# Performance work log

Measured on AMD Instinct MI355X. Metric: run time of the kernel, lower is better.

## Reference

```python
import jax, jax.numpy as jnp
import numpy as np

B, F, S = 2, 512, 1024
E = 4
I = 1024          # intermediate = 2 * features
K = 3             # conv kernel size
INIT_SCALE = 1.0
EPS = 1e-5
SLOPE = 0.02


def setup_inputs() -> dict:
    key = jax.random.key(0)
    k = jax.random.split(key, 6)
    inp = jax.random.normal(k[0], (B, F, S), jnp.float32)
    divisor = (jnp.arange(S, dtype=jnp.float32) + 1.0).reshape(1, 1, S)
    w0_gate = jax.random.normal(k[1], (E, F, 1), jnp.float32) * (F ** -0.5)
    w0 = jax.random.normal(k[2], (E, F, 3 * I), jnp.float32) * (F ** -0.5)
    w1 = jax.random.normal(k[3], (3 * I, I, K), jnp.float32) * ((I * K) ** -0.5)
    w2_gate = jax.random.normal(k[4], (E, I, 1), jnp.float32) * (I ** -0.5)
    w2 = jax.random.normal(k[5], (E, I, F), jnp.float32) * (I ** -0.5)
    return {"inp": inp, "divisor": divisor, "w0_gate": w0_gate, "w0": w0,
            "w1": w1, "w2_gate": w2_gate, "w2": w2}


def _norm(x):
    # channel norm over dim 1: subtract mean, divide by scaled L2 norm
    x = x - jnp.mean(x, axis=1, keepdims=True)
    n = jnp.sqrt(jnp.sum(x * x, axis=1, keepdims=True)) * (x.shape[1] ** -0.5)
    return x / (n + EPS)


def _moe(x, gate, w):
    # x: [B,F,S]; gate: [E,F,1]; w: [E,F,D]
    logits = jnp.einsum('bfs,ef->bes', x, gate[:, :, 0])          # [B,E,S]
    gates = jax.nn.softmax(logits, axis=1)
    idx = jnp.argmax(logits, axis=1)                              # [B,S]
    one_hot = jax.nn.one_hot(idx, w.shape[0], dtype=x.dtype)      # [B,S,E]
    # straight-through gumbel-style gate: hard one-hot fwd, soft grad
    gumbel = jnp.transpose(one_hot, (0, 2, 1)) - jax.lax.stop_gradient(gates) + gates  # [B,E,S]
    xs = jnp.transpose(x, (0, 2, 1))                              # [B,S,F]
    out = jnp.zeros((x.shape[0], x.shape[2], w.shape[2]), x.dtype)
    for e in range(w.shape[0]):  # small fixed expert count
        mask = one_hot[:, :, e][:, :, None]                       # [B,S,1]
        out = out + mask * ((xs * gumbel[:, e, :, None]) @ w[e])
    loss = jnp.sum(jnp.mean(gates, axis=(0, 2)) * jnp.mean(one_hot, axis=(0, 1)))
    return loss, jnp.transpose(out, (0, 2, 1))                    # [B,D,S]


def _conv1d(x, w, causal_pad):
    if causal_pad and w.shape[-1] > 1:
        x = jnp.pad(x, ((0, 0), (0, 0), (w.shape[-1] - 1, 0)))
    return jax.lax.conv_general_dilated(
        x, w, window_strides=(1,), padding='VALID',
        dimension_numbers=('NCH', 'OIH', 'NCH'), feature_group_count=1)


def reference(inp, divisor, w0_gate, w0, w1, w2_gate, w2):
    loss0, h = _moe(inp, w0_gate, w0)                 # [B,3I,S]
    depth, scale, shift = jnp.split(h, 3, axis=1)     # each [B,I,S]
    cum = jnp.cumsum(depth, axis=-1)
    h = jax.nn.leaky_relu(_norm(cum / divisor * scale + shift), SLOPE)
    h = _conv1d(h, w1, causal_pad=True)               # [B,3I,S]
    s0, s1, sh = jnp.split(h, 3, axis=1)
    h = jax.nn.leaky_relu(_norm(s0 * s1 + sh), SLOPE)
    loss1, out = _moe(h, w2_gate, w2)                 # [B,F,S]
    return out * INIT_SCALE, loss0 + loss1
```

## Files before the change

### kernel.cpp

```cpp
#include <hip/hip_runtime.h>
#include <hip/hip_bf16.h>

#define SDIM 1024

typedef float f32x4 __attribute__((ext_vector_type(4)));
typedef short short8 __attribute__((ext_vector_type(8)));

__device__ __forceinline__ unsigned short f2bf(float f) {
    __hip_bfloat16 h = __float2bfloat16(f);
    return *reinterpret_cast<unsigned short*>(&h);
}
__device__ __forceinline__ float bf2f(unsigned short u) {
    return __uint_as_float(((unsigned int)u) << 16);
}

__global__ void init_acc_kernel(float* acc) {
    int t = threadIdx.x;
    if (t < 16) acc[t] = 0.0f;
}

__global__ __launch_bounds__(256) void transpose_cvt_split(
    const float* __restrict__ in, unsigned short* __restrict__ oh,
    unsigned short* __restrict__ ol, int R, int C, size_t sliceStride)
{
    __shared__ float t[32][33];
    int slice = blockIdx.z;
    int c0 = blockIdx.x * 32, r0 = blockIdx.y * 32;
    int tid = threadIdx.x;
    int cc = tid & 31, r8 = tid >> 5;
    const float* ip = in + slice * sliceStride;
    #pragma unroll
    for (int k = 0; k < 4; ++k) {
        int r = r8 + k * 8;
        t[r][cc] = ip[(size_t)(r0 + r) * C + c0 + cc];
    }
    __syncthreads();
    #pragma unroll
    for (int k = 0; k < 4; ++k) {
        int rr = r8 + k * 8;
        float v = t[cc][rr];
        unsigned short hi = f2bf(v);
        unsigned short lo = f2bf(v - bf2f(hi));
        size_t o = slice * sliceStride + (size_t)(c0 + rr) * R + r0 + cc;
        oh[o] = hi; ol[o] = lo;
    }
}

__global__ __launch_bounds__(256) void transpose_cvt(
    const float* __restrict__ in, unsigned short* __restrict__ out,
    int R, int C, size_t sliceStride)
{
    __shared__ float t[32][33];
    int slice = blockIdx.z;
    int c0 = blockIdx.x * 32, r0 = blockIdx.y * 32;
    int tid = threadIdx.x;
    int cc = tid & 31, r8 = tid >> 5;
    const float* ip = in + slice * sliceStride;
    unsigned short* op = out + slice * sliceStride;
    #pragma unroll
    for (int k = 0; k < 4; ++k) {
        int r = r8 + k * 8;
        t[r][cc] = ip[(size_t)(r0 + r) * C + c0 + cc];
    }
    __syncthreads();
    #pragma unroll
    for (int k = 0; k < 4; ++k) {
        int rr = r8 + k * 8;
        op[(size_t)(c0 + rr) * R + r0 + cc] = f2bf(t[cc][rr]);
    }
}

__global__ __launch_bounds__(256) void w1cvt_split_kernel(
    const float* __restrict__ w1, unsigned short* __restrict__ wh,
    unsigned short* __restrict__ wl)
{
    int t = blockIdx.x * 256 + threadIdx.x;
    int o = t >> 10, i = t & 1023;
    const float* p = w1 + (size_t)o * 3072 + i * 3;
    #pragma unroll
    for (int k = 0; k < 3; ++k) {
        float v = p[k];
        unsigned short hi = f2bf(v);
        unsigned short lo = f2bf(v - bf2f(hi));
        size_t off = (size_t)k * 3145728 + (size_t)o * 1024 + i;
        wh[off] = hi; wl[off] = lo;
    }
}

__global__ __launch_bounds__(256) void gate_kernel(
    const float* __restrict__ x, const float* __restrict__ wg,
    int* __restrict__ idx, float* __restrict__ acc, int accBase)
{
    __shared__ float wgs[4 * 512];
    __shared__ float part[32][4][9];
    __shared__ float la[8];
    int tid = threadIdx.x;
    if (tid < 8) la[tid] = 0.f;
    for (int l = tid; l < 2048; l += 256) wgs[l] = wg[l];
    __syncthreads();
    int t0 = blockIdx.x * 8;
    int b = t0 >> 10, s0 = t0 & 1023;
    int sl = tid & 7, fg = tid >> 3;
    float l0 = 0.f, l1 = 0.f, l2 = 0.f, l3 = 0.f;
    for (int f = fg; f < 512; f += 32) {
        float xv = x[((size_t)b * 512 + f) * SDIM + s0 + sl];
        l0 += xv * wgs[f];
        l1 += xv * wgs[512 + f];
        l2 += xv * wgs[1024 + f];
        l3 += xv * wgs[1536 + f];
    }
    part[fg][0][sl] = l0; part[fg][1][sl] = l1;
    part[fg][2][sl] = l2; part[fg][3][sl] = l3;
    __syncthreads();
    for (int h = 16; h >= 1; h >>= 1) {
        if (fg < h) {
            #pragma unroll
            for (int e = 0; e < 4; ++e) part[fg][e][sl] += part[fg + h][e][sl];
        }
        __syncthreads();
    }
    if (fg == 0) {
        float L[4] = {part[0][0][sl], part[0][1][sl], part[0][2][sl], part[0][3][sl]};
        float m = fmaxf(fmaxf(L[0], L[1]), fmaxf(L[2], L[3]));
        float e0 = expf(L[0] - m), e1 = expf(L[1] - m), e2 = expf(L[2] - m), e3 = expf(L[3] - m);
        float inv = 1.0f / (e0 + e1 + e2 + e3);
        int best = 0; float bv = L[0];
        if (L[1] > bv) { bv = L[1]; best = 1; }
        if (L[2] > bv) { bv = L[2]; best = 2; }
        if (L[3] > bv) { bv = L[3]; best = 3; }
        idx[t0 + sl] = best;
        atomicAdd(&la[0], e0 * inv);
        atomicAdd(&la[1], e1 * inv);
        atomicAdd(&la[2], e2 * inv);
        atomicAdd(&la[3], e3 * inv);
        atomicAdd(&la[4 + best], 1.0f);
    }
    __syncthreads();
    if (tid < 8) atomicAdd(&acc[accBase + tid], la[tid]);
}

__global__ __launch_bounds__(1024) void sort_kernel(
    const int* __restrict__ idx, int* __restrict__ perm, int* __restrict__ eSorted)
{
    int b = blockIdx.x;
    int tid = threadIdx.x;
    int lane = tid & 63, w = tid >> 6;
    int e = idx[(b << 10) + tid];
    __shared__ int wcnt[16][4];
    __shared__ int woff[16][4];
    int r = 0;
    unsigned long long lt = (1ull << lane) - 1ull;
    #pragma unroll
    for (int eo = 0; eo < 4; ++eo) {
        unsigned long long m = __ballot(e == eo);
        if (lane == 0) wcnt[w][eo] = __popcll(m);
        if (e == eo) r = __popcll(m & lt);
    }
    __syncthreads();
    if (tid == 0) {
        int baseAcc = 0;
        for (int eo = 0; eo < 4; ++eo)
            for (int ww = 0; ww < 16; ++ww) { woff[ww][eo] = baseAcc; baseAcc += wcnt[ww][eo]; }
    }
    __syncthreads();
    int pos = woff[w][e] + r;
    perm[(b << 10) + pos] = tid;
    eSorted[(b << 10) + pos] = e;
}

__global__ __launch_bounds__(256) void moe_split_kernel(
    const unsigned short* __restrict__ base, unsigned int XH, unsigned int XL,
    unsigned int WH, unsigned int WL,
    const int* __restrict__ perm, const int* __restrict__ eSorted,
    float* __restrict__ out, int Fdim, int Ddim)
{
    __shared__ unsigned short lds[768 * 32];
    int id = blockIdx.x;
    int chunk = gridDim.x >> 3;
    int wg = (id & 7) * chunk + (id >> 3);
    int t0 = (wg & 15) * 128;
    int d0 = (wg >> 4) * 64;
    int b = t0 >> 10, s0 = t0 & 1023;
    int tid = threadIdx.x;
    int lane = tid & 63;
    int lm = lane & 15, q = lane >> 4;
    int wid = tid >> 6;
    int wm = (wid >> 1) * 32, wn = (wid & 1) * 64;

    unsigned int goH[6], goL[6];
    int ldH[6], ldL[6];
    #pragma unroll
    for (int t = 0; t < 6; ++t) {
        int cl = tid + t * 256;
        int row = cl >> 2, p = cl & 3;
        int rh, rl;
        unsigned int off;
        if (row < 128) {
            int tj = perm[(b << 10) + s0 + row];
            off = (unsigned int)(((b << 10) + tj) * Fdim + p * 8);
            goH[t] = XH + off; goL[t] = XL + off;
            rh = row; rl = row + 128;
        } else {
            int R = row - 128;
            int e = R >> 6, dl = R & 63;
            off = (unsigned int)((e * Ddim + d0 + dl) * Fdim + p * 8);
            goH[t] = WH + off; goL[t] = WL + off;
            rh = 256 + R; rl = 512 + R;
        }
        ldH[t] = rh * 32 + ((p ^ ((rh >> 1) & 3)) << 3);
        ldL[t] = rl * 32 + ((p ^ ((rl >> 1) & 3)) << 3);
    }

    int bofH[4], bofL[4], aofH[4][2], aofL[4][2];
    #pragma unroll
    for (int fn = 0; fn < 4; ++fn) {
        int rh = wn + fn * 16 + lm, rl = rh + 128;
        bofH[fn] = rh * 32 + ((q ^ ((rh >> 1) & 3)) << 3);
        bofL[fn] = rl * 32 + ((q ^ ((rl >> 1) & 3)) << 3);
    }
    #pragma unroll
    for (int e = 0; e < 4; ++e)
        #pragma unroll
        for (int fm = 0; fm < 2; ++fm) {
            int rh = 256 + e * 64 + wm + fm * 16 + lm;
            int rl = rh + 256;
            aofH[e][fm] = rh * 32 + ((q ^ ((rh >> 1) & 3)) << 3);
            aofL[e][fm] = rl * 32 + ((q ^ ((rl >> 1) & 3)) << 3);
        }

    int eidx[4], sv[4];
    #pragma unroll
    for (int fn = 0; fn < 4; ++fn) {
        int sl = (b << 10) + s0 + wn + fn * 16 + lm;
        eidx[fn] = eSorted[sl];
        sv[fn]   = perm[sl];
    }
    bool presF[4][4], presE[4];
    #pragma unroll
    for (int e = 0; e < 4; ++e) {
        presE[e] = false;
        #pragma unroll
        for (int fn = 0; fn < 4; ++fn) {
            presF[e][fn] = __any(eidx[fn] == e);
            presE[e] = presE[e] || presF[e][fn];
        }
    }

    f32x4 acc[2][4];
    #pragma unroll
    for (int fm = 0; fm < 2; ++fm)
        #pragma unroll
        for (int fn = 0; fn < 4; ++fn)
            acc[fm][fn] = (f32x4){0.f, 0.f, 0.f, 0.f};

    const short8 z = {0, 0, 0, 0, 0, 0, 0, 0};

    for (int f0 = 0; f0 < Fdim; f0 += 32) {
        short8 vh[6], vl[6];
        #pragma unroll
        for (int t = 0; t < 6; ++t) vh[t] = *(const short8*)(base + goH[t] + f0);
        #pragma unroll
        for (int t = 0; t < 6; ++t) vl[t] = *(const short8*)(base + goL[t] + f0);
        __syncthreads();
        #pragma unroll
        for (int t = 0; t < 6; ++t) {
            *(short8*)(lds + ldH[t]) = vh[t];
            *(short8*)(lds + ldL[t]) = vl[t];
        }
        __syncthreads();

        short8 bh[4], bl[4];
        #pragma unroll
        for (int fn = 0; fn < 4; ++fn) {
            bh[fn] = *(const short8*)(lds + bofH[fn]);
            bl[fn] = *(const short8*)(lds + bofL[fn]);
        }
        #pragma unroll
        for (int e = 0; e < 4; ++e) {
            if (presE[e]) {
                short8 ah[2], al[2];
                #pragma unroll
                for (int fm = 0; fm < 2; ++fm) {
                    ah[fm] = *(const short8*)(lds + aofH[e][fm]);
                    al[fm] = *(const short8*)(lds + aofL[e][fm]);
                }
                #pragma unroll
                for (int fn = 0; fn < 4; ++fn) {
                    if (presF[e][fn]) {
                        short8 bmH = (eidx[fn] == e) ? bh[fn] : z;
                        short8 bmL = (eidx[fn] == e) ? bl[fn] : z;
                        #pragma unroll
                        for (int fm = 0; fm < 2; ++fm) {
                            acc[fm][fn] = __builtin_amdgcn_mfma_f32_16x16x32_bf16(ah[fm], bmH, acc[fm][fn], 0, 0, 0);
                            acc[fm][fn] = __builtin_amdgcn_mfma_f32_16x16x32_bf16(ah[fm], bmL, acc[fm][fn], 0, 0, 0);
                            acc[fm][fn] = __builtin_amdgcn_mfma_f32_16x16x32_bf16(al[fm], bmH, acc[fm][fn], 0, 0, 0);
                        }
                    }
                }
            }
        }
    }

    #pragma unroll
    for (int fm = 0; fm < 2; ++fm)
        #pragma unroll
        for (int fn = 0; fn < 4; ++fn) {
            int d = d0 + wm + fm * 16 + q * 4;
            float* op = out + ((size_t)b * Ddim + d) * SDIM + sv[fn];
            #pragma unroll
            for (int r = 0; r < 4; ++r)
                op[(size_t)r * SDIM] = acc[fm][fn][r];
        }
}

__global__ __launch_bounds__(256) void conv_split_kernel(
    const unsigned short* __restrict__ base, unsigned int GH, unsigned int GL,
    unsigned int WH, unsigned int WL, float* __restrict__ co)
{
    __shared__ unsigned short lds[864 * 32];
    int id = blockIdx.x;
    int wg = (id & 7) * 64 + (id >> 3);
    int t0 = (wg & 15) * 128;
    int o0 = (wg >> 4) * 96;
    int b = t0 >> 10, s0 = t0 & 1023;
    int tid = threadIdx.x;
    int lane = tid & 63;
    int lm = lane & 15, q = lane >> 4;
    int wid = tid >> 6;
    int wm = (wid >> 1) * 48, wn = (wid & 1) * 64;

    unsigned int goH[7], goL[7];
    int ldH[7], ldL[7], act[7];
    #pragma unroll
    for (int t = 0; t < 7; ++t) {
        int cl = tid + t * 256;
        int row = cl >> 2, p = cl & 3;
        int rh, rl;
        if (row < 144) { rh = row; rl = row + 144; }
        else { int R = row - 144; rh = 288 + R; rl = 576 + R; }
        ldH[t] = rh * 32 + ((p ^ ((rh >> 1) & 3)) << 3);
        ldL[t] = rl * 32 + ((p ^ ((rl >> 1) & 3)) << 3);
        act[t] = 0; goH[t] = 0; goL[t] = 0;
        if (cl < 1728) {
            if (row < 144) {
                int s = s0 - 2 + row;
                if (s >= 0 && s < 1024) {
                    act[t] = 1;
                    unsigned int off = ((unsigned int)((b << 10) + s) << 10) + p * 8;
                    goH[t] = GH + off; goL[t] = GL + off;
                } else if (s < 0) {
                    act[t] = 2;
                }
            } else {
                int R = row - 144;
                int k = R / 96, ol = R - k * 96;
                act[t] = 1;
                unsigned int off = (unsigned int)k * 3145728u + ((unsigned int)(o0 + ol) << 10) + p * 8;
                goH[t] = WH + off; goL[t] = WL + off;
            }
        }
    }

    int aofH[3][3], aofL[3][3], bofH[3][4], bofL[3][4];
    #pragma unroll
    for (int k = 0; k < 3; ++k) {
        #pragma unroll
        for (int fm = 0; fm < 3; ++fm) {
            int R = k * 96 + wm + fm * 16 + lm;
            int rh = 288 + R, rl = 576 + R;
            aofH[k][fm] = rh * 32 + ((q ^ ((rh >> 1) & 3)) << 3);
            aofL[k][fm] = rl * 32 + ((q ^ ((rl >> 1) & 3)) << 3);
        }
        #pragma unroll
        for (int fn = 0; fn < 4; ++fn) {
            int rh = wn + fn * 16 + lm + k;
            int rl = rh + 144;
            bofH[k][fn] = rh * 32 + ((q ^ ((rh >> 1) & 3)) << 3);
            bofL[k][fn] = rl * 32 + ((q ^ ((rl >> 1) & 3)) << 3);
        }
    }

    f32x4 acc[3][4];
    #pragma unroll
    for (int fm = 0; fm < 3; ++fm)
        #pragma unroll
        for (int fn = 0; fn < 4; ++fn)
            acc[fm][fn] = (f32x4){0.f, 0.f, 0.f, 0.f};

    const short8 z = {0, 0, 0, 0, 0, 0, 0, 0};

    #pragma unroll
    for (int t = 0; t < 7; ++t)
        if (act[t] == 2) { *(short8*)(lds + ldH[t]) = z; *(short8*)(lds + ldL[t]) = z; }

    for (int i0 = 0; i0 < 1024; i0 += 32) {
        short8 vh[7], vl[7];
        #pragma unroll
        for (int t = 0; t < 7; ++t) vh[t] = (act[t] == 1) ? *(const short8*)(base + goH[t] + i0) : z;
        #pragma unroll
        for (int t = 0; t < 7; ++t) vl[t] = (act[t] == 1) ? *(const short8*)(base + goL[t] + i0) : z;
        __syncthreads();
        #pragma unroll
        for (int t = 0; t < 7; ++t)
            if (act[t] == 1) {
                *(short8*)(lds + ldH[t]) = vh[t];
                *(short8*)(lds + ldL[t]) = vl[t];
            }
        __syncthreads();

        #pragma unroll
        for (int k = 0; k < 3; ++k) {
            short8 ah[3], al[3], bh[4], bl[4];
            #pragma unroll
            for (int fm = 0; fm < 3; ++fm) {
                ah[fm] = *(const short8*)(lds + aofH[k][fm]);
                al[fm] = *(const short8*)(lds + aofL[k][fm]);
            }
            #pragma unroll
            for (int fn = 0; fn < 4; ++fn) {
                bh[fn] = *(const short8*)(lds + bofH[k][fn]);
                bl[fn] = *(const short8*)(lds + bofL[k][fn]);
            }
            #pragma unroll
            for (int fm = 0; fm < 3; ++fm)
                #pragma unroll
                for (int fn = 0; fn < 4; ++fn) {
                    acc[fm][fn] = __builtin_amdgcn_mfma_f32_16x16x32_bf16(ah[fm], bh[fn], acc[fm][fn], 0, 0, 0);
                    acc[fm][fn] = __builtin_amdgcn_mfma_f32_16x16x32_bf16(ah[fm], bl[fn], acc[fm][fn], 0, 0, 0);
                    acc[fm][fn] = __builtin_amdgcn_mfma_f32_16x16x32_bf16(al[fm], bh[fn], acc[fm][fn], 0, 0, 0);
                }
        }
    }

    #pragma unroll
    for (int fm = 0; fm < 3; ++fm)
        #pragma unroll
        for (int fn = 0; fn < 4; ++fn) {
            int o = o0 + wm + fm * 16 + q * 4;
            int s = s0 + wn + fn * 16 + lm;
            float* op = co + ((size_t)b * 3072 + o) * SDIM + s;
            #pragma unroll
            for (int r = 0; r < 4; ++r)
                op[(size_t)r * SDIM] = acc[fm][fn][r];
        }
}

__global__ __launch_bounds__(256) void moe_kernel(
    const unsigned short* __restrict__ xT, const unsigned short* __restrict__ wT,
    const int* __restrict__ perm, const int* __restrict__ eSorted,
    float* __restrict__ out, int Fdim, int Ddim)
{
    __shared__ unsigned short lds[384 * 32];
    int id = blockIdx.x;
    int chunk = gridDim.x >> 3;
    int wg = (id & 7) * chunk + (id >> 3);
    int t0 = (wg & 15) * 128;
    int d0 = (wg >> 4) * 64;
    int b = t0 >> 10, s0 = t0 & 1023;
    int tid = threadIdx.x;
    int lane = tid & 63, wid = tid >> 6;
    int lm = lane & 15, q = lane >> 4;
    int wm = (wid >> 1) * 32, wn = (wid & 1) * 64;

    const unsigned short* gsrc[6];
    int ldst[6];
    #pragma unroll
    for (int t = 0; t < 6; ++t) {
        int cl = tid + t * 256;
        int row = cl >> 2, p = cl & 3;
        int pr;
        if (row < 128) {
            int tj = perm[(b << 10) + s0 + row];
            gsrc[t] = xT + (size_t)((b << 10) + tj) * Fdim + p * 8;
            pr = row;
        } else {
            int R = row - 128;
            int e = R >> 6, dl = R & 63;
            gsrc[t] = wT + (size_t)(e * Ddim + d0 + dl) * Fdim + p * 8;
            pr = 128 + R;
        }
        ldst[t] = pr * 32 + ((p ^ ((pr >> 1) & 3)) << 3);
    }

    int bof[4], aof[4][2];
    #pragma unroll
    for (int fn = 0; fn < 4; ++fn) {
        int row = wn + fn * 16 + lm;
        bof[fn] = row * 32 + ((q ^ ((row >> 1) & 3)) << 3);
    }
    #pragma unroll
    for (int e = 0; e < 4; ++e)
        #pragma unroll
        for (int fm = 0; fm < 2; ++fm) {
            int R = 128 + e * 64 + wm + fm * 16 + lm;
            aof[e][fm] = R * 32 + ((q ^ ((R >> 1) & 3)) << 3);
        }

    int eidx[4], sv[4];
    #pragma unroll
    for (int fn = 0; fn < 4; ++fn) {
        int sl = (b << 10) + s0 + wn + fn * 16 + lm;
        eidx[fn] = eSorted[sl];
        sv[fn]   = perm[sl];
    }
    bool presF[4][4], presE[4];
    #pragma unroll
    for (int e = 0; e < 4; ++e) {
        presE[e] = false;
        #pragma unroll
        for (int fn = 0; fn < 4; ++fn) {
            presF[e][fn] = __any(eidx[fn] == e);
            presE[e] = presE[e] || presF[e][fn];
        }
    }

    f32x4 acc[2][4];
    #pragma unroll
    for (int fm = 0; fm < 2; ++fm)
        #pragma unroll
        for (int fn = 0; fn < 4; ++fn)
            acc[fm][fn] = (f32x4){0.f, 0.f, 0.f, 0.f};

    const short8 z = {0, 0, 0, 0, 0, 0, 0, 0};

    for (int f0 = 0; f0 < Fdim; f0 += 32) {
        short8 v[6];
        #pragma unroll
        for (int t = 0; t < 6; ++t)
            v[t] = *(const short8*)(gsrc[t] + f0);
        __syncthreads();
        #pragma unroll
        for (int t = 0; t < 6; ++t)
            *(short8*)(lds + ldst[t]) = v[t];
        __syncthreads();

        short8 bf[4];
        #pragma unroll
        for (int fn = 0; fn < 4; ++fn)
            bf[fn] = *(const short8*)(lds + bof[fn]);
        #pragma unroll
        for (int e = 0; e < 4; ++e) {
            if (presE[e]) {
                short8 af[2];
                #pragma unroll
                for (int fm = 0; fm < 2; ++fm)
                    af[fm] = *(const short8*)(lds + aof[e][fm]);
                #pragma unroll
                for (int fn = 0; fn < 4; ++fn) {
                    if (presF[e][fn]) {
                        short8 bm = (eidx[fn] == e) ? bf[fn] : z;
                        #pragma unroll
                        for (int fm = 0; fm < 2; ++fm)
                            acc[fm][fn] = __builtin_amdgcn_mfma_f32_16x16x32_bf16(af[fm], bm, acc[fm][fn], 0, 0, 0);
                    }
                }
            }
        }
    }

    #pragma unroll
    for (int fm = 0; fm < 2; ++fm)
        #pragma unroll
        for (int fn = 0; fn < 4; ++fn) {
            int d = d0 + wm + fm * 16 + q * 4;
            float* op = out + ((size_t)b * Ddim + d) * SDIM + sv[fn];
            #pragma unroll
            for (int r = 0; r < 4; ++r)
                op[(size_t)r * SDIM] = acc[fm][fn][r];
        }
}

__global__ __launch_bounds__(256) void cumsum_affine_kernel(
    const float* __restrict__ h1, const float* __restrict__ divisor,
    float* __restrict__ y)
{
    int r = blockIdx.x;
    int b = r >> 10, i = r & 1023;
    const float4* dp = (const float4*)(h1 + ((size_t)b * 3072 + i) * SDIM);
    const float4* sp = (const float4*)(h1 + ((size_t)b * 3072 + 1024 + i) * SDIM);
    const float4* hp = (const float4*)(h1 + ((size_t)b * 3072 + 2048 + i) * SDIM);
    int tid = threadIdx.x;
    float4 v = dp[tid];
    float c0 = v.x, c1 = c0 + v.y, c2 = c1 + v.z, c3 = c2 + v.w;
    __shared__ float part[256];
    part[tid] = c3;
    __syncthreads();
    for (int off = 1; off < 256; off <<= 1) {
        float p = (tid >= off) ? part[tid - off] : 0.f;
        __syncthreads();
        part[tid] += p;
        __syncthreads();
    }
    float base = part[tid] - c3;
    float4 sc = sp[tid], sh = hp[tid];
    float4 dv = ((const float4*)divisor)[tid];
    float4 o;
    o.x = (base + c0) / dv.x * sc.x + sh.x;
    o.y = (base + c1) / dv.y * sc.y + sh.y;
    o.z = (base + c2) / dv.z * sc.z + sh.z;
    o.w = (base + c3) / dv.w * sc.w + sh.w;
    ((float4*)(y + ((size_t)b * 1024 + i) * SDIM))[tid] = o;
}

__global__ __launch_bounds__(256) void norm0_kernel(
    const float* __restrict__ g, unsigned short* __restrict__ oh,
    unsigned short* __restrict__ ol)
{
    int blk = blockIdx.x;
    int b = blk >> 7;
    int s0 = (blk & 127) * 8;
    int tid = threadIdx.x;
    int sg = tid & 7, grp = tid >> 3;
    int s = s0 + sg;
    const float* bp = g + ((size_t)b * 1024) * SDIM + s;
    float v[32];
    float sum = 0.f, ssq = 0.f;
    #pragma unroll
    for (int j = 0; j < 32; ++j) {
        float x = bp[(size_t)(grp * 32 + j) * SDIM];
        v[j] = x; sum += x; ssq += x * x;
    }
    __shared__ float rs[32][8], rq[32][8], stat[2][8];
    rs[grp][sg] = sum; rq[grp][sg] = ssq;
    __syncthreads();
    for (int h = 16; h >= 1; h >>= 1) {
        if (grp < h) { rs[grp][sg] += rs[grp + h][sg]; rq[grp][sg] += rq[grp + h][sg]; }
        __syncthreads();
    }
    if (grp == 0) {
        float S1 = rs[0][sg], S2 = rq[0][sg];
        float mean = S1 * (1.0f / 1024.0f);
        float ssc = fmaxf(S2 - 1024.0f * mean * mean, 0.0f);
        stat[0][sg] = mean;
        stat[1][sg] = 1.0f / (sqrtf(ssc) * (1.0f / 32.0f) + 1e-5f);
    }
    __syncthreads();
    float mean = stat[0][sg], inv = stat[1][sg];
    size_t tbase = (((size_t)b << 10) + s) * 1024 + grp * 32;
    #pragma unroll
    for (int j0 = 0; j0 < 32; j0 += 4) {
        unsigned short uh[4], ul[4];
        #pragma unroll
        for (int jj = 0; jj < 4; ++jj) {
            float o = (v[j0 + jj] - mean) * inv;
            o = (o >= 0.f) ? o : 0.02f * o;
            uh[jj] = f2bf(o);
            ul[jj] = f2bf(o - bf2f(uh[jj]));
        }
        *(ushort4*)(oh + tbase + j0) = (ushort4){uh[0], uh[1], uh[2], uh[3]};
        *(ushort4*)(ol + tbase + j0) = (ushort4){ul[0], ul[1], ul[2], ul[3]};
    }
}

__global__ __launch_bounds__(256) void normgate_kernel(
    const float* __restrict__ h1, const float* __restrict__ wg,
    unsigned short* __restrict__ outT, int* __restrict__ idx, float* __restrict__ acc)
{
    int blk = blockIdx.x;
    int b = blk >> 7;
    int s0 = (blk & 127) * 8;
    int tid = threadIdx.x;
    int sg = tid & 7, grp = tid >> 3;
    int s = s0 + sg;
    const float* bp = h1 + ((size_t)b * 3072) * SDIM + s;
    float v[32];
    float sum = 0.f, ssq = 0.f;
    #pragma unroll
    for (int j = 0; j < 32; ++j) {
        int i = grp * 32 + j;
        float a  = bp[(size_t)i * SDIM];
        float m2 = bp[(size_t)(1024 + i) * SDIM];
        float d2 = bp[(size_t)(2048 + i) * SDIM];
        float x = a * m2 + d2;
        v[j] = x; sum += x; ssq += x * x;
    }
    __shared__ float rs[32][8], rq[32][8], stat[2][8];
    rs[grp][sg] = sum; rq[grp][sg] = ssq;
    __syncthreads();
    for (int h = 16; h >= 1; h >>= 1) {
        if (grp < h) { rs[grp][sg] += rs[grp + h][sg]; rq[grp][sg] += rq[grp + h][sg]; }
        __syncthreads();
    }
    if (grp == 0) {
        float S1 = rs[0][sg], S2 = rq[0][sg];
        float mean = S1 * (1.0f / 1024.0f);
        float ssc = fmaxf(S2 - 1024.0f * mean * mean, 0.0f);
        stat[0][sg] = mean;
        stat[1][sg] = 1.0f / (sqrtf(ssc) * (1.0f / 32.0f) + 1e-5f);
    }
    __syncthreads();
    float mean = stat[0][sg], inv = stat[1][sg];
    float l0 = 0.f, l1 = 0.f, l2 = 0.f, l3 = 0.f;
    size_t tbase = (((size_t)b << 10) + s) * 1024 + grp * 32;
    #pragma unroll
    for (int j0 = 0; j0 < 32; j0 += 4) {
        unsigned short u[4];
        #pragma unroll
        for (int jj = 0; jj < 4; ++jj) {
            int i = grp * 32 + j0 + jj;
            float o = (v[j0 + jj] - mean) * inv;
            o = (o >= 0.f) ? o : 0.02f * o;
            u[jj] = f2bf(o);
            l0 += o * wg[i];
            l1 += o * wg[1024 + i];
            l2 += o * wg[2048 + i];
            l3 += o * wg[3072 + i];
        }
        *(ushort4*)(outT + tbase + j0) = (ushort4){u[0], u[1], u[2], u[3]};
    }
    __shared__ float pl[4][32][8];
    __shared__ float la[8];
    pl[0][grp][sg] = l0; pl[1][grp][sg] = l1;
    pl[2][grp][sg] = l2; pl[3][grp][sg] = l3;
    if (tid < 8) la[tid] = 0.f;
    __syncthreads();
    for (int h = 16; h >= 1; h >>= 1) {
        if (grp < h) {
            #pragma unroll
            for (int e = 0; e < 4; ++e) pl[e][grp][sg] += pl[e][grp + h][sg];
        }
        __syncthreads();
    }
    if (grp == 0) {
        float L[4] = {pl[0][0][sg], pl[1][0][sg], pl[2][0][sg], pl[3][0][sg]};
        float m = fmaxf(fmaxf(L[0], L[1]), fmaxf(L[2], L[3]));
        float e0 = expf(L[0] - m), e1 = expf(L[1] - m), e2 = expf(L[2] - m), e3 = expf(L[3] - m);
        float invs = 1.0f / (e0 + e1 + e2 + e3);
        int best = 0; float bv = L[0];
        if (L[1] > bv) { bv = L[1]; best = 1; }
        if (L[2] > bv) { bv = L[2]; best = 2; }
        if (L[3] > bv) { bv = L[3]; best = 3; }
        idx[(b << 10) + s] = best;
        atomicAdd(&la[0], e0 * invs);
        atomicAdd(&la[1], e1 * invs);
        atomicAdd(&la[2], e2 * invs);
        atomicAdd(&la[3], e3 * invs);
        atomicAdd(&la[4 + best], 1.0f);
    }
    __syncthreads();
    if (tid < 8) atomicAdd(&acc[8 + tid], la[tid]);
}

__global__ void loss_kernel(const float* __restrict__ acc, float* __restrict__ out) {
    if (threadIdx.x == 0) {
        float l = 0.f;
        for (int e = 0; e < 4; ++e)
            l += acc[e] * acc[4 + e] + acc[8 + e] * acc[12 + e];
        out[2 * 512 * 1024] = l * (1.0f / (2048.0f * 2048.0f));
    }
}

extern "C" void kernel_launch(void* const* d_in, const int* in_sizes, int n_in,
                              void* d_out, int out_size, void* d_ws, size_t ws_size,
                              hipStream_t stream) {
    const float* inp     = (const float*)d_in[0];
    const float* divisor = (const float*)d_in[1];
    const float* w0_gate = (const float*)d_in[2];
    const float* w0      = (const float*)d_in[3];
    const float* w1      = (const float*)d_in[4];
    const float* w2_gate = (const float*)d_in[5];
    const float* w2      = (const float*)d_in[6];
    float* out = (float*)d_out;
    (void)in_sizes; (void)n_in; (void)out_size; (void)ws_size;

    char* ws = (char*)d_ws;
    const unsigned short* base = (const unsigned short*)ws;

    float* h1            = (float*)(ws + 0);
    float* g             = (float*)(ws + 25165824);
    unsigned short* gT1h = (unsigned short*)(ws + 33554432);
    unsigned short* gT1l = (unsigned short*)(ws + 37748736);
    unsigned short* w1Th = (unsigned short*)(ws + 41943040);
    unsigned short* w1Tl = (unsigned short*)(ws + 60817408);
    unsigned short* xTh  = (unsigned short*)(ws + 79691776);
    unsigned short* xTl  = (unsigned short*)(ws + 81788928);
    unsigned short* w0Th = (unsigned short*)(ws + 83886080);
    unsigned short* w0Tl = (unsigned short*)(ws + 96468992);
    unsigned short* gT2  = (unsigned short*)(ws + 79691776);
    unsigned short* w2T  = (unsigned short*)(ws + 83886080);
    int* idx1            = (int*)(ws + 109051904);
    int* idx2            = (int*)(ws + 109060096);
    float* acc           = (float*)(ws + 109068288);
    int* perm1           = (int*)(ws + 109076480);
    int* eSort1          = (int*)(ws + 109084672);
    int* perm2           = (int*)(ws + 109092864);
    int* eSort2          = (int*)(ws + 109101056);

    const unsigned int GT1H = 16777216u, GT1L = 18874368u;
    const unsigned int W1TH = 20971520u, W1TL = 30408704u;
    const unsigned int XTH  = 39845888u, XTL  = 40894464u;
    const unsigned int W0TH = 41943040u, W0TL = 48234496u;

    init_acc_kernel<<<1, 16, 0, stream>>>(acc);

    transpose_cvt_split<<<dim3(32, 16, 2), 256, 0, stream>>>(inp, xTh, xTl, 512, 1024, (size_t)512 * 1024);
    transpose_cvt_split<<<dim3(96, 16, 4), 256, 0, stream>>>(w0, w0Th, w0Tl, 512, 3072, (size_t)512 * 3072);
    w1cvt_split_kernel<<<12288, 256, 0, stream>>>(w1, w1Th, w1Tl);

    gate_kernel<<<256, 256, 0, stream>>>(inp, w0_gate, idx1, acc, 0);
    sort_kernel<<<2, 1024, 0, stream>>>(idx1, perm1, eSort1);
    moe_split_kernel<<<768, 256, 0, stream>>>(base, XTH, XTL, W0TH, W0TL, perm1, eSort1, h1, 512, 3072);

    transpose_cvt<<<dim3(16, 32, 4), 256, 0, stream>>>(w2, w2T, 1024, 512, (size_t)1024 * 512);

    cumsum_affine_kernel<<<2048, 256, 0, stream>>>(h1, divisor, g);
    norm0_kernel<<<256, 256, 0, stream>>>(g, gT1h, gT1l);
    conv_split_kernel<<<512, 256, 0, stream>>>(base, GT1H, GT1L, W1TH, W1TL, h1);
    normgate_kernel<<<256, 256, 0, stream>>>(h1, w2_gate, gT2, idx2, acc);

    sort_kernel<<<2, 1024, 0, stream>>>(idx2, perm2, eSort2);
    moe_kernel<<<128, 256, 0, stream>>>(gT2, w2T, perm2, eSort2, out, 1024, 512);
    loss_kernel<<<1, 64, 0, stream>>>(acc, out);
}
```

Measured before the change: 288.3 us.

## Load weight operands directly from global memory instead of staging through LDS

In the MoE and conv GEMM kernels, weight (A) fragments are now read straight from global memory into registers each k-step rather than cooperatively staged into shared memory. Only the activation (B) tile goes through LDS, which shrinks LDS use and the per-iteration staging stores. Each wave now loads its own weight rows, so rows shared across waves are fetched redundantly and the loads are uncoalesced short8 reads whose latency sits in the MFMA loop without prefetch.

```diff
diff --git a/kernel.cpp b/kernel.cpp
--- a/kernel.cpp
+++ b/kernel.cpp
@@ -174,7 +174,7 @@
     const int* __restrict__ perm, const int* __restrict__ eSorted,
     float* __restrict__ out, int Fdim, int Ddim)
 {
-    __shared__ unsigned short lds[768 * 32];
+    __shared__ unsigned short lds[256 * 32];
     int id = blockIdx.x;
     int chunk = gridDim.x >> 3;
     int wg = (id & 7) * chunk + (id >> 3);
@@ -187,46 +187,31 @@
     int wid = tid >> 6;
     int wm = (wid >> 1) * 32, wn = (wid & 1) * 64;
 
-    unsigned int goH[6], goL[6];
-    int ldH[6], ldL[6];
-    #pragma unroll
-    for (int t = 0; t < 6; ++t) {
+    unsigned int goH[2], goL[2];
+    int ldst[2];
+    #pragma unroll
+    for (int t = 0; t < 2; ++t) {
         int cl = tid + t * 256;
         int row = cl >> 2, p = cl & 3;
-        int rh, rl;
-        unsigned int off;
-        if (row < 128) {
-            int tj = perm[(b << 10) + s0 + row];
-            off = (unsigned int)(((b << 10) + tj) * Fdim + p * 8);
-            goH[t] = XH + off; goL[t] = XL + off;
-            rh = row; rl = row + 128;
-        } else {
-            int R = row - 128;
-            int e = R >> 6, dl = R & 63;
-            off = (unsigned int)((e * Ddim + d0 + dl) * Fdim + p * 8);
-            goH[t] = WH + off; goL[t] = WL + off;
-            rh = 256 + R; rl = 512 + R;
-        }
-        ldH[t] = rh * 32 + ((p ^ ((rh >> 1) & 3)) << 3);
-        ldL[t] = rl * 32 + ((p ^ ((rl >> 1) & 3)) << 3);
-    }
-
-    int bofH[4], bofL[4], aofH[4][2], aofL[4][2];
+        int tj = perm[(b << 10) + s0 + row];
+        unsigned int off = (unsigned int)(((b << 10) + tj) * Fdim + p * 8);
+        goH[t] = XH + off; goL[t] = XL + off;
+        ldst[t] = row * 32 + ((p ^ ((row >> 1) & 3)) << 3);
+    }
+
+    int bofH[4];
     #pragma unroll
     for (int fn = 0; fn < 4; ++fn) {
-        int rh = wn + fn * 16 + lm, rl = rh + 128;
+        int rh = wn + fn * 16 + lm;
         bofH[fn] = rh * 32 + ((q ^ ((rh >> 1) & 3)) << 3);
-        bofL[fn] = rl * 32 + ((q ^ ((rl >> 1) & 3)) << 3);
-    }
+    }
+    unsigned int aof[4][2];
     #pragma unroll
     for (int e = 0; e < 4; ++e)
         #pragma unroll
-        for (int fm = 0; fm < 2; ++fm) {
-            int rh = 256 + e * 64 + wm + fm * 16 + lm;
-            int rl = rh + 256;
-            aofH[e][fm] = rh * 32 + ((q ^ ((rh >> 1) & 3)) << 3);
-            aofL[e][fm] = rl * 32 + ((q ^ ((rl >> 1) & 3)) << 3);
-        }
+        for (int fm = 0; fm < 2; ++fm)
+            aof[e][fm] = WH + (unsigned int)((e * Ddim + d0 + wm + fm * 16 + lm) * Fdim + q * 8);
+    const unsigned int WLD = WL - WH;
 
     int eidx[4], sv[4];
     #pragma unroll
@@ -256,16 +241,17 @@
     const short8 z = {0, 0, 0, 0, 0, 0, 0, 0};
 
     for (int f0 = 0; f0 < Fdim; f0 += 32) {
-        short8 vh[6], vl[6];
-        #pragma unroll
-        for (int t = 0; t < 6; ++t) vh[t] = *(const short8*)(base + goH[t] + f0);
-        #pragma unroll
-        for (int t = 0; t < 6; ++t) vl[t] = *(const short8*)(base + goL[t] + f0);
-        __syncthreads();
-        #pragma unroll
-        for (int t = 0; t < 6; ++t) {
-            *(short8*)(lds + ldH[t]) = vh[t];
-            *(short8*)(lds + ldL[t]) = vl[t];
+        short8 vh[2], vl[2];
+        #pragma unroll
+        for (int t = 0; t < 2; ++t) {
+            vh[t] = *(const short8*)(base + goH[t] + f0);
+            vl[t] = *(const short8*)(base + goL[t] + f0);
+        }
+        __syncthreads();
+        #pragma unroll
+        for (int t = 0; t < 2; ++t) {
+            *(short8*)(lds + ldst[t]) = vh[t];
+            *(short8*)(lds + ldst[t] + 4096) = vl[t];
         }
         __syncthreads();
 
@@ -273,7 +259,7 @@
         #pragma unroll
         for (int fn = 0; fn < 4; ++fn) {
             bh[fn] = *(const short8*)(lds + bofH[fn]);
-            bl[fn] = *(const short8*)(lds + bofL[fn]);
+            bl[fn] = *(const short8*)(lds + bofH[fn] + 4096);
         }
         #pragma unroll
         for (int e = 0; e < 4; ++e) {
@@ -281,8 +267,8 @@
                 short8 ah[2], al[2];
                 #pragma unroll
                 for (int fm = 0; fm < 2; ++fm) {
-                    ah[fm] = *(const short8*)(lds + aofH[e][fm]);
-                    al[fm] = *(const short8*)(lds + aofL[e][fm]);
+                    ah[fm] = *(const short8*)(base + aof[e][fm] + f0);
+                    al[fm] = *(const short8*)(base + aof[e][fm] + WLD + f0);
                 }
                 #pragma unroll
                 for (int fn = 0; fn < 4; ++fn) {
@@ -317,7 +303,7 @@
     const unsigned short* __restrict__ base, unsigned int GH, unsigned int GL,
     unsigned int WH, unsigned int WL, float* __restrict__ co)
 {
-    __shared__ unsigned short lds[864 * 32];
+    __shared__ unsigned short lds[288 * 32];
     int id = blockIdx.x;
     int wg = (id & 7) * 64 + (id >> 3);
     int t0 = (wg & 15) * 128;
@@ -329,56 +315,43 @@
     int wid = tid >> 6;
     int wm = (wid >> 1) * 48, wn = (wid & 1) * 64;
 
-    unsigned int goH[7], goL[7];
-    int ldH[7], ldL[7], act[7];
-    #pragma unroll
-    for (int t = 0; t < 7; ++t) {
+    unsigned int goH[3], goL[3];
+    int ldH[3], act[3];
+    #pragma unroll
+    for (int t = 0; t < 3; ++t) {
         int cl = tid + t * 256;
         int row = cl >> 2, p = cl & 3;
-        int rh, rl;
-        if (row < 144) { rh = row; rl = row + 144; }
-        else { int R = row - 144; rh = 288 + R; rl = 576 + R; }
-        ldH[t] = rh * 32 + ((p ^ ((rh >> 1) & 3)) << 3);
-        ldL[t] = rl * 32 + ((p ^ ((rl >> 1) & 3)) << 3);
+        ldH[t] = row * 32 + ((p ^ ((row >> 1) & 3)) << 3);
         act[t] = 0; goH[t] = 0; goL[t] = 0;
-        if (cl < 1728) {
-            if (row < 144) {
-                int s = s0 - 2 + row;
-                if (s >= 0 && s < 1024) {
-                    act[t] = 1;
-                    unsigned int off = ((unsigned int)((b << 10) + s) << 10) + p * 8;
-                    goH[t] = GH + off; goL[t] = GL + off;
-                } else if (s < 0) {
-                    act[t] = 2;
-                }
-            } else {
-                int R = row - 144;
-                int k = R / 96, ol = R - k * 96;
+        if (cl < 576) {
+            int s = s0 - 2 + row;
+            if (s >= 0 && s < 1024) {
                 act[t] = 1;
-                unsigned int off = (unsigned int)k * 3145728u + ((unsigned int)(o0 + ol) << 10) + p * 8;
-                goH[t] = WH + off; goL[t] = WL + off;
+                unsigned int off = ((unsigned int)((b << 10) + s) << 10) + p * 8;
+                goH[t] = GH + off; goL[t] = GL + off;
+            } else if (s < 0) {
+                act[t] = 2;
             }
         }
     }
 
-    int aofH[3][3], aofL[3][3], bofH[3][4], bofL[3][4];
-    #pragma unroll
-    for (int k = 0; k < 3; ++k) {
-        #pragma unroll
-        for (int fm = 0; fm < 3; ++fm) {
-            int R = k * 96 + wm + fm * 16 + lm;
-            int rh = 288 + R, rl = 576 + R;
-            aofH[k][fm] = rh * 32 + ((q ^ ((rh >> 1) & 3)) << 3);
-            aofL[k][fm] = rl * 32 + ((q ^ ((rl >> 1) & 3)) << 3);
-        }
+    int bofH[3][4];
+    #pragma unroll
+    for (int k = 0; k < 3; ++k)
         #pragma unroll
         for (int fn = 0; fn < 4; ++fn) {
             int rh = wn + fn * 16 + lm + k;
-            int rl = rh + 144;
             bofH[k][fn] = rh * 32 + ((q ^ ((rh >> 1) & 3)) << 3);
-            bofL[k][fn] = rl * 32 + ((q ^ ((rl >> 1) & 3)) << 3);
-        }
-    }
+        }
+
+    unsigned int aof[3][3];
+    #pragma unroll
+    for (int k = 0; k < 3; ++k)
+        #pragma unroll
+        for (int fm = 0; fm < 3; ++fm)
+            aof[k][fm] = WH + (unsigned int)k * 3145728u
+                       + ((unsigned int)(o0 + wm + fm * 16 + lm) << 10) + q * 8;
+    const unsigned int WLD = WL - WH;
 
     f32x4 acc[3][4];
     #pragma unroll
@@ -390,21 +363,25 @@
     const short8 z = {0, 0, 0, 0, 0, 0, 0, 0};
 
     #pragma unroll
-    for (int t = 0; t < 7; ++t)
-        if (act[t] == 2) { *(short8*)(lds + ldH[t]) = z; *(short8*)(lds + ldL[t]) = z; }
+    for (int t = 0; t < 3; ++t)
+        if (act[t] == 2) {
+            *(short8*)(lds + ldH[t]) = z;
+            *(short8*)(lds + ldH[t] + 4608) = z;
+        }
 
     for (int i0 = 0; i0 < 1024; i0 += 32) {
-        short8 vh[7], vl[7];
-        #pragma unroll
-        for (int t = 0; t < 7; ++t) vh[t] = (act[t] == 1) ? *(const short8*)(base + goH[t] + i0) : z;
-        #pragma unroll
-        for (int t = 0; t < 7; ++t) vl[t] = (act[t] == 1) ? *(const short8*)(base + goL[t] + i0) : z;
-        __syncthreads();
-        #pragma unroll
-        for (int t = 0; t < 7; ++t)
+        short8 vh[3], vl[3];
+        #pragma unroll
+        for (int t = 0; t < 3; ++t) {
+            vh[t] = (act[t] == 1) ? *(const short8*)(base + goH[t] + i0) : z;
+            vl[t] = (act[t] == 1) ? *(const short8*)(base + goL[t] + i0) : z;
+        }
+        __syncthreads();
+        #pragma unroll
+        for (int t = 0; t < 3; ++t)
             if (act[t] == 1) {
                 *(short8*)(lds + ldH[t]) = vh[t];
-                *(short8*)(lds + ldL[t]) = vl[t];
+                *(short8*)(lds + ldH[t] + 4608) = vl[t];
             }
         __syncthreads();
 
@@ -413,13 +390,13 @@
             short8 ah[3], al[3], bh[4], bl[4];
             #pragma unroll
             for (int fm = 0; fm < 3; ++fm) {
-                ah[fm] = *(const short8*)(lds + aofH[k][fm]);
-                al[fm] = *(const short8*)(lds + aofL[k][fm]);
+                ah[fm] = *(const short8*)(base + aof[k][fm] + i0);
+                al[fm] = *(const short8*)(base + aof[k][fm] + WLD + i0);
             }
             #pragma unroll
             for (int fn = 0; fn < 4; ++fn) {
                 bh[fn] = *(const short8*)(lds + bofH[k][fn]);
-                bl[fn] = *(const short8*)(lds + bofL[k][fn]);
+                bl[fn] = *(const short8*)(lds + bofH[k][fn] + 4608);
             }
             #pragma unroll
             for (int fm = 0; fm < 3; ++fm)
@@ -450,7 +427,7 @@
     const int* __restrict__ perm, const int* __restrict__ eSorted,
     float* __restrict__ out, int Fdim, int Ddim)
 {
-    __shared__ unsigned short lds[384 * 32];
+    __shared__ unsigned short lds[128 * 32];
     int id = blockIdx.x;
     int chunk = gridDim.x >> 3;
     int wg = (id & 7) * chunk + (id >> 3);
@@ -462,39 +439,29 @@
     int lm = lane & 15, q = lane >> 4;
     int wm = (wid >> 1) * 32, wn = (wid & 1) * 64;
 
-    const unsigned short* gsrc[6];
-    int ldst[6];
-    #pragma unroll
-    for (int t = 0; t < 6; ++t) {
+    const unsigned short* gsrc[2];
+    int ldst[2];
+    #pragma unroll
+    for (int t = 0; t < 2; ++t) {
         int cl = tid + t * 256;
         int row = cl >> 2, p = cl & 3;
-        int pr;
-        if (row < 128) {
-            int tj = perm[(b << 10) + s0 + row];
-            gsrc[t] = xT + (size_t)((b << 10) + tj) * Fdim + p * 8;
-            pr = row;
-        } else {
-            int R = row - 128;
-            int e = R >> 6, dl = R & 63;
-            gsrc[t] = wT + (size_t)(e * Ddim + d0 + dl) * Fdim + p * 8;
-            pr = 128 + R;
-        }
-        ldst[t] = pr * 32 + ((p ^ ((pr >> 1) & 3)) << 3);
-    }
-
-    int bof[4], aof[4][2];
+        int tj = perm[(b << 10) + s0 + row];
+        gsrc[t] = xT + (size_t)((b << 10) + tj) * Fdim + p * 8;
+        ldst[t] = row * 32 + ((p ^ ((row >> 1) & 3)) << 3);
+    }
+
+    int bof[4];
     #pragma unroll
     for (int fn = 0; fn < 4; ++fn) {
         int row = wn + fn * 16 + lm;
         bof[fn] = row * 32 + ((q ^ ((row >> 1) & 3)) << 3);
     }
+    const unsigned short* aptr[4][2];
     #pragma unroll
     for (int e = 0; e < 4; ++e)
         #pragma unroll
-        for (int fm = 0; fm < 2; ++fm) {
-            int R = 128 + e * 64 + wm + fm * 16 + lm;
-            aof[e][fm] = R * 32 + ((q ^ ((R >> 1) & 3)) << 3);
-        }
+        for (int fm = 0; fm < 2; ++fm)
+            aptr[e][fm] = wT + (size_t)(e * Ddim + d0 + wm + fm * 16 + lm) * Fdim + q * 8;
 
     int eidx[4], sv[4];
     #pragma unroll
@@ -524,13 +491,13 @@
     const short8 z = {0, 0, 0, 0, 0, 0, 0, 0};
 
     for (int f0 = 0; f0 < Fdim; f0 += 32) {
-        short8 v[6];
-        #pragma unroll
-        for (int t = 0; t < 6; ++t)
+        short8 v[2];
+        #pragma unroll
+        for (int t = 0; t < 2; ++t)
             v[t] = *(const short8*)(gsrc[t] + f0);
         __syncthreads();
         #pragma unroll
-        for (int t = 0; t < 6; ++t)
+        for (int t = 0; t < 2; ++t)
             *(short8*)(lds + ldst[t]) = v[t];
         __syncthreads();
 
@@ -544,7 +511,7 @@
                 short8 af[2];
                 #pragma unroll
                 for (int fm = 0; fm < 2; ++fm)
-                    af[fm] = *(const short8*)(lds + aof[e][fm]);
+                    af[fm] = *(const short8*)(aptr[e][fm] + f0);
                 #pragma unroll
                 for (int fn = 0; fn < 4; ++fn) {
                     if (presF[e][fn]) {
```

Result: slower. 328.3 us (+13.9%).

## Stage GEMM tiles via direct global-to-LDS loads and skip absent expert weights

Applied to the files above, without the earlier changes.

Replaces the register-staged global loads plus LDS stores in the three MoE/conv GEMM kernels with the global_load_lds builtin, which writes 16-byte segments straight into LDS using a segment layout that keeps the XOR swizzle. The MoE kernels also skip loading weight rows for experts outside the sorted tile's expert range. The conv kernel's left-padding rows now read from a zeroed workspace buffer set by a memset, which removes the conditional zero path. This is meant to cut VGPR pressure and LDS-store instructions, at the cost of one extra memset and reliance on the sorted expert order.

```diff
diff --git a/kernel.cpp b/kernel.cpp
--- a/kernel.cpp
+++ b/kernel.cpp
@@ -12,6 +12,10 @@
 }
 __device__ __forceinline__ float bf2f(unsigned short u) {
     return __uint_as_float(((unsigned int)u) << 16);
+}
+__device__ __forceinline__ void gload_lds16(const unsigned short* g, unsigned short* l) {
+    __builtin_amdgcn_global_load_lds((const __attribute__((address_space(1))) void*)g,
+                                     (__attribute__((address_space(3))) void*)l, 16, 0, 0);
 }
 
 __global__ void init_acc_kernel(float* acc) {
@@ -187,37 +191,42 @@
     int wid = tid >> 6;
     int wm = (wid >> 1) * 32, wn = (wid & 1) * 64;
 
-    unsigned int goH[6], goL[6];
-    int ldH[6], ldL[6];
-    #pragma unroll
-    for (int t = 0; t < 6; ++t) {
-        int cl = tid + t * 256;
-        int row = cl >> 2, p = cl & 3;
-        int rh, rl;
-        unsigned int off;
-        if (row < 128) {
-            int tj = perm[(b << 10) + s0 + row];
-            off = (unsigned int)(((b << 10) + tj) * Fdim + p * 8);
-            goH[t] = XH + off; goL[t] = XL + off;
-            rh = row; rl = row + 128;
+    int eLo = eSorted[(b << 10) + s0];
+    int eHi = eSorted[(b << 10) + s0 + 127];
+
+    unsigned int gofs[12];
+    int lofs[12], doSeg[12];
+    #pragma unroll
+    for (int j = 0; j < 12; ++j) {
+        int seg = wid + 4 * j;
+        int row = seg * 16 + (lane >> 2);
+        int slot = lane & 3;
+        int c = slot ^ ((row >> 1) & 3);
+        unsigned int src;
+        int act = 1;
+        if (row < 256) {
+            int gr = (row < 128) ? row : row - 128;
+            unsigned int hb = (row < 128) ? XH : XL;
+            int tj = perm[(b << 10) + s0 + gr];
+            src = hb + (unsigned int)(((b << 10) + tj) * Fdim) + c * 8;
         } else {
-            int R = row - 128;
-            int e = R >> 6, dl = R & 63;
-            off = (unsigned int)((e * Ddim + d0 + dl) * Fdim + p * 8);
-            goH[t] = WH + off; goL[t] = WL + off;
-            rh = 256 + R; rl = 512 + R;
-        }
-        ldH[t] = rh * 32 + ((p ^ ((rh >> 1) & 3)) << 3);
-        ldL[t] = rl * 32 + ((p ^ ((rl >> 1) & 3)) << 3);
-    }
-
-    int bofH[4], bofL[4], aofH[4][2], aofL[4][2];
+            int R = row - 256;
+            unsigned int hb = WH;
+            if (R >= 256) { R -= 256; hb = WL; }
+            int e = R >> 6;
+            act = (e >= eLo && e <= eHi) ? 1 : 0;
+            src = hb + (unsigned int)((e * Ddim + d0 + (R & 63)) * Fdim) + c * 8;
+        }
+        gofs[j] = src; lofs[j] = seg * 512 + lane * 8; doSeg[j] = act;
+    }
+
+    int bofH[4];
     #pragma unroll
     for (int fn = 0; fn < 4; ++fn) {
-        int rh = wn + fn * 16 + lm, rl = rh + 128;
+        int rh = wn + fn * 16 + lm;
         bofH[fn] = rh * 32 + ((q ^ ((rh >> 1) & 3)) << 3);
-        bofL[fn] = rl * 32 + ((q ^ ((rl >> 1) & 3)) << 3);
-    }
+    }
+    int aofH[4][2], aofL[4][2];
     #pragma unroll
     for (int e = 0; e < 4; ++e)
         #pragma unroll
@@ -256,24 +265,17 @@
     const short8 z = {0, 0, 0, 0, 0, 0, 0, 0};
 
     for (int f0 = 0; f0 < Fdim; f0 += 32) {
-        short8 vh[6], vl[6];
-        #pragma unroll
-        for (int t = 0; t < 6; ++t) vh[t] = *(const short8*)(base + goH[t] + f0);
-        #pragma unroll
-        for (int t = 0; t < 6; ++t) vl[t] = *(const short8*)(base + goL[t] + f0);
-        __syncthreads();
-        #pragma unroll
-        for (int t = 0; t < 6; ++t) {
-            *(short8*)(lds + ldH[t]) = vh[t];
-            *(short8*)(lds + ldL[t]) = vl[t];
-        }
+        __syncthreads();
+        #pragma unroll
+        for (int j = 0; j < 12; ++j)
+            if (doSeg[j]) gload_lds16(base + gofs[j] + f0, lds + lofs[j]);
         __syncthreads();
 
         short8 bh[4], bl[4];
         #pragma unroll
         for (int fn = 0; fn < 4; ++fn) {
             bh[fn] = *(const short8*)(lds + bofH[fn]);
-            bl[fn] = *(const short8*)(lds + bofL[fn]);
+            bl[fn] = *(const short8*)(lds + bofH[fn] + 4096);
         }
         #pragma unroll
         for (int e = 0; e < 4; ++e) {
@@ -315,7 +317,7 @@
 
 __global__ __launch_bounds__(256) void conv_split_kernel(
     const unsigned short* __restrict__ base, unsigned int GH, unsigned int GL,
-    unsigned int WH, unsigned int WL, float* __restrict__ co)
+    unsigned int WH, unsigned int WL, unsigned int ZB, float* __restrict__ co)
 {
     __shared__ unsigned short lds[864 * 32];
     int id = blockIdx.x;
@@ -329,35 +331,34 @@
     int wid = tid >> 6;
     int wm = (wid >> 1) * 48, wn = (wid & 1) * 64;
 
-    unsigned int goH[7], goL[7];
-    int ldH[7], ldL[7], act[7];
-    #pragma unroll
-    for (int t = 0; t < 7; ++t) {
-        int cl = tid + t * 256;
-        int row = cl >> 2, p = cl & 3;
-        int rh, rl;
-        if (row < 144) { rh = row; rl = row + 144; }
-        else { int R = row - 144; rh = 288 + R; rl = 576 + R; }
-        ldH[t] = rh * 32 + ((p ^ ((rh >> 1) & 3)) << 3);
-        ldL[t] = rl * 32 + ((p ^ ((rl >> 1) & 3)) << 3);
-        act[t] = 0; goH[t] = 0; goL[t] = 0;
-        if (cl < 1728) {
-            if (row < 144) {
-                int s = s0 - 2 + row;
-                if (s >= 0 && s < 1024) {
-                    act[t] = 1;
-                    unsigned int off = ((unsigned int)((b << 10) + s) << 10) + p * 8;
-                    goH[t] = GH + off; goL[t] = GL + off;
-                } else if (s < 0) {
-                    act[t] = 2;
-                }
+    unsigned int gofs[14];
+    int lofs[14];
+    int nseg = (wid < 2) ? 14 : 13;
+    #pragma unroll
+    for (int j = 0; j < 14; ++j) {
+        int seg = wid + 4 * j;
+        gofs[j] = ZB; lofs[j] = 0;
+        if (seg < 54) {
+            int row = seg * 16 + (lane >> 2);
+            int slot = lane & 3;
+            int c = slot ^ ((row >> 1) & 3);
+            unsigned int src;
+            if (row < 288) {
+                int gr = (row < 144) ? row : row - 144;
+                unsigned int hb = (row < 144) ? GH : GL;
+                int s = s0 - 2 + gr;
+                if (s < 0) src = ZB + c * 8;
+                else { if (s > 1023) s = 1023;
+                       src = hb + ((unsigned int)((b << 10) + s) << 10) + c * 8; }
             } else {
-                int R = row - 144;
+                int R = row - 288;
+                unsigned int hb = WH;
+                if (R >= 288) { R -= 288; hb = WL; }
                 int k = R / 96, ol = R - k * 96;
-                act[t] = 1;
-                unsigned int off = (unsigned int)k * 3145728u + ((unsigned int)(o0 + ol) << 10) + p * 8;
-                goH[t] = WH + off; goL[t] = WL + off;
+                src = hb + (unsigned int)k * 3145728u + ((unsigned int)(o0 + ol) << 10) + c * 8;
             }
+            gofs[j] = src;
+            lofs[j] = seg * 512 + lane * 8;
         }
     }
 
@@ -387,25 +388,11 @@
         for (int fn = 0; fn < 4; ++fn)
             acc[fm][fn] = (f32x4){0.f, 0.f, 0.f, 0.f};
 
-    const short8 z = {0, 0, 0, 0, 0, 0, 0, 0};
-
-    #pragma unroll
-    for (int t = 0; t < 7; ++t)
-        if (act[t] == 2) { *(short8*)(lds + ldH[t]) = z; *(short8*)(lds + ldL[t]) = z; }
-
     for (int i0 = 0; i0 < 1024; i0 += 32) {
-        short8 vh[7], vl[7];
-        #pragma unroll
-        for (int t = 0; t < 7; ++t) vh[t] = (act[t] == 1) ? *(const short8*)(base + goH[t] + i0) : z;
-        #pragma unroll
-        for (int t = 0; t < 7; ++t) vl[t] = (act[t] == 1) ? *(const short8*)(base + goL[t] + i0) : z;
-        __syncthreads();
-        #pragma unroll
-        for (int t = 0; t < 7; ++t)
-            if (act[t] == 1) {
-                *(short8*)(lds + ldH[t]) = vh[t];
-                *(short8*)(lds + ldL[t]) = vl[t];
-            }
+        __syncthreads();
+        #pragma unroll
+        for (int j = 0; j < 14; ++j)
+            if (j < nseg) gload_lds16(base + gofs[j] + i0, lds + lofs[j]);
         __syncthreads();
 
         #pragma unroll
@@ -462,24 +449,29 @@
     int lm = lane & 15, q = lane >> 4;
     int wm = (wid >> 1) * 32, wn = (wid & 1) * 64;
 
+    int eLo = eSorted[(b << 10) + s0];
+    int eHi = eSorted[(b << 10) + s0 + 127];
+
     const unsigned short* gsrc[6];
-    int ldst[6];
-    #pragma unroll
-    for (int t = 0; t < 6; ++t) {
-        int cl = tid + t * 256;
-        int row = cl >> 2, p = cl & 3;
-        int pr;
+    int lofs[6], doSeg[6];
+    #pragma unroll
+    for (int j = 0; j < 6; ++j) {
+        int seg = wid + 4 * j;
+        int row = seg * 16 + (lane >> 2);
+        int slot = lane & 3;
+        int c = slot ^ ((row >> 1) & 3);
+        int act = 1;
+        const unsigned short* src;
         if (row < 128) {
             int tj = perm[(b << 10) + s0 + row];
-            gsrc[t] = xT + (size_t)((b << 10) + tj) * Fdim + p * 8;
-            pr = row;
+            src = xT + (size_t)((b << 10) + tj) * Fdim + c * 8;
         } else {
             int R = row - 128;
-            int e = R >> 6, dl = R & 63;
-            gsrc[t] = wT + (size_t)(e * Ddim + d0 + dl) * Fdim + p * 8;
-            pr = 128 + R;
-        }
-        ldst[t] = pr * 32 + ((p ^ ((pr >> 1) & 3)) << 3);
+            int e = R >> 6;
+            act = (e >= eLo && e <= eHi) ? 1 : 0;
+            src = wT + (size_t)(e * Ddim + d0 + (R & 63)) * Fdim + c * 8;
+        }
+        gsrc[j] = src; lofs[j] = seg * 512 + lane * 8; doSeg[j] = act;
     }
 
     int bof[4], aof[4][2];
@@ -524,14 +516,10 @@
     const short8 z = {0, 0, 0, 0, 0, 0, 0, 0};
 
     for (int f0 = 0; f0 < Fdim; f0 += 32) {
-        short8 v[6];
-        #pragma unroll
-        for (int t = 0; t < 6; ++t)
-            v[t] = *(const short8*)(gsrc[t] + f0);
-        __syncthreads();
-        #pragma unroll
-        for (int t = 0; t < 6; ++t)
-            *(short8*)(lds + ldst[t]) = v[t];
+        __syncthreads();
+        #pragma unroll
+        for (int j = 0; j < 6; ++j)
+            if (doSeg[j]) gload_lds16(gsrc[j] + f0, lds + lofs[j]);
         __syncthreads();
 
         short8 bf[4];
@@ -785,13 +773,16 @@
     int* eSort1          = (int*)(ws + 109084672);
     int* perm2           = (int*)(ws + 109092864);
     int* eSort2          = (int*)(ws + 109101056);
+    char* zbuf           = ws + 109109248;
 
     const unsigned int GT1H = 16777216u, GT1L = 18874368u;
     const unsigned int W1TH = 20971520u, W1TL = 30408704u;
     const unsigned int XTH  = 39845888u, XTL  = 40894464u;
     const unsigned int W0TH = 41943040u, W0TL = 48234496u;
+    const unsigned int ZB   = 54554624u;
 
     init_acc_kernel<<<1, 16, 0, stream>>>(acc);
+    hipMemsetAsync(zbuf, 0, 4096, stream);
 
     transpose_cvt_split<<<dim3(32, 16, 2), 256, 0, stream>>>(inp, xTh, xTl, 512, 1024, (size_t)512 * 1024);
     transpose_cvt_split<<<dim3(96, 16, 4), 256, 0, stream>>>(w0, w0Th, w0Tl, 512, 3072, (size_t)512 * 3072);
@@ -805,7 +796,7 @@
 
     cumsum_affine_kernel<<<2048, 256, 0, stream>>>(h1, divisor, g);
     norm0_kernel<<<256, 256, 0, stream>>>(g, gT1h, gT1l);
-    conv_split_kernel<<<512, 256, 0, stream>>>(base, GT1H, GT1L, W1TH, W1TL, h1);
+    conv_split_kernel<<<512, 256, 0, stream>>>(base, GT1H, GT1L, W1TH, W1TL, ZB, h1);
     normgate_kernel<<<256, 256, 0, stream>>>(h1, w2_gate, gT2, idx2, acc);
 
     sort_kernel<<<2, 1024, 0, stream>>>(idx2, perm2, eSort2);
```

Result: faster. 266.2 us (-7.7%).
